# Performance work log

Hardware: AMD Instinct MI355X
Metric: run time of the kernel (lower is better)

## Reference

```python
import jax, jax.numpy as jnp
import numpy as np

D = 1024      # d_model
H = 4096      # d_hidden (attention head dim AND mlp width in this module)
V = 32000     # d_vocab
L = 4         # num_blocks
B = 2         # batch
S = 2048      # seq len == max_seq_length
SCALE = 1.0 / float(np.sqrt(D))  # note: original scales by sqrt(d_model), not sqrt(d_hidden)
EPS = 1e-5


def setup_inputs() -> dict:
    key = jax.random.key(0)
    ks = jax.random.split(key, 18)
    s = 0.02
    tokens = jax.random.randint(ks[0], (B, S), 0, V)
    tok_emb = jax.random.normal(ks[1], (V, D), dtype=jnp.float32) * s
    pos_emb = jax.random.normal(ks[2], (1, S, D), dtype=jnp.float32) * s
    # stacked per-block params [L, ...]
    Wq = jax.random.normal(ks[3], (L, D, H), dtype=jnp.float32) * s
    bq = jnp.zeros((L, H), jnp.float32)
    Wk = jax.random.normal(ks[4], (L, D, H), dtype=jnp.float32) * s
    bk = jnp.zeros((L, H), jnp.float32)
    Wv = jax.random.normal(ks[5], (L, D, H), dtype=jnp.float32) * s
    bv = jnp.zeros((L, H), jnp.float32)
    Wo = jax.random.normal(ks[6], (L, H, D), dtype=jnp.float32) * s
    bo = jnp.zeros((L, D), jnp.float32)
    Wup = jax.random.normal(ks[7], (L, D, H), dtype=jnp.float32) * s
    bup = jnp.zeros((L, H), jnp.float32)
    Wdn = jax.random.normal(ks[8], (L, H, D), dtype=jnp.float32) * s
    bdn = jnp.zeros((L, D), jnp.float32)
    ln_g = jnp.ones((D,), jnp.float32)
    ln_b = jnp.zeros((D,), jnp.float32)
    Wu = jax.random.normal(ks[9], (D, V), dtype=jnp.float32) * s
    bu = jnp.zeros((V,), jnp.float32)
    return dict(tokens=tokens, tok_emb=tok_emb, pos_emb=pos_emb,
                Wq=Wq, bq=bq, Wk=Wk, bk=bk, Wv=Wv, bv=bv, Wo=Wo, bo=bo,
                Wup=Wup, bup=bup, Wdn=Wdn, bdn=bdn,
                ln_g=ln_g, ln_b=ln_b, Wu=Wu, bu=bu)


def _forward(tokens, tok_emb, pos_emb, Wq, bq, Wk, bk, Wv, bv, Wo, bo,
             Wup, bup, Wdn, bdn, ln_g, ln_b, Wu, bu):
    seq = tokens.shape[1]
    x = tok_emb[tokens] + pos_emb[:, :seq, :]            # [B,S,D]
    mask = jnp.triu(jnp.full((seq, seq), -jnp.inf, jnp.float32), k=1)  # strict upper -inf

    def block(x, p):
        wq, _bq, wk, _bk, wv, _bv, wo, _bo, wup, _bup, wdn, _bdn = p
        Q = x @ wq + _bq                                  # [B,S,H]
        K = x @ wk + _bk
        Vv = x @ wv + _bv
        scores = jnp.einsum('bqh,bkh->bqk', Q, K) * SCALE + mask
        attn = jax.nn.softmax(scores, axis=-1)            # [B,S,S]
        x = x + jnp.einsum('bqk,bkh->bqh', attn, Vv) @ wo + _bo
        h = jax.nn.relu(x @ wup + _bup)
        x = x + h @ wdn + _bdn
        return x, None

    x, _ = jax.lax.scan(block, x, (Wq, bq, Wk, bk, Wv, bv, Wo, bo, Wup, bup, Wdn, bdn))
    mu = jnp.mean(x, axis=-1, keepdims=True)
    var = jnp.mean((x - mu) ** 2, axis=-1, keepdims=True)
    x = (x - mu) / jnp.sqrt(var + EPS) * ln_g + ln_b
    logits = x @ Wu + bu                                  # [B,S,V]
    return logits


def reference(tokens, tok_emb, pos_emb, Wq, bq, Wk, bk, Wv, bv, Wo, bo,
              Wup, bup, Wdn, bdn, ln_g, ln_b, Wu, bu):
    return _forward(tokens, tok_emb, pos_emb, Wq, bq, Wk, bk, Wv, bv, Wo, bo,
                    Wup, bup, Wdn, bdn, ln_g, ln_b, Wu, bu)
```

## Files before the change

kernel.cpp:

```cpp
#include <hip/hip_runtime.h>
#include <hip/hip_bf16.h>

typedef __bf16 bf16_t;
typedef __attribute__((ext_vector_type(8))) __bf16 bf16x8;
typedef __attribute__((ext_vector_type(4))) float f32x4;

#define D_MODEL 1024
#define H_DIM   4096
#define VOCAB   32000
#define NBLK    4
#define BATCH   2
#define SEQ     2048
#define NTOK    (BATCH*SEQ)
#define SCALE_QK (1.0f/32.0f)
#define LN_EPS  1e-5f

#define BM 128
#define BN 128
#define BK 32
#define GROUP_M 8
#define NXCD 8

__device__ __forceinline__ void gload16(const bf16_t* g, bf16_t* l) {
    __builtin_amdgcn_global_load_lds(
        (const __attribute__((address_space(1))) void*)g,
        (__attribute__((address_space(3))) void*)l,
        16, 0, 0);
}

__global__ void embed_kernel(const int* __restrict__ tokens,
                             const float* __restrict__ tok_emb,
                             const float* __restrict__ pos_emb,
                             float* __restrict__ x, bf16_t* __restrict__ xb) {
    int row = blockIdx.x;
    int s   = row & (SEQ - 1);
    int tok = tokens[row];
    const float* te = tok_emb + (size_t)tok * D_MODEL;
    const float* pe = pos_emb + (size_t)s * D_MODEL;
    int d = threadIdx.x * 4;
    float4 a = *(const float4*)(te + d);
    float4 p = *(const float4*)(pe + d);
    float4 r; r.x = a.x + p.x; r.y = a.y + p.y; r.z = a.z + p.z; r.w = a.w + p.w;
    *(float4*)(x + (size_t)row * D_MODEL + d) = r;
    union { bf16_t h[4]; unsigned long long u; } pk;
    pk.h[0] = (bf16_t)r.x; pk.h[1] = (bf16_t)r.y; pk.h[2] = (bf16_t)r.z; pk.h[3] = (bf16_t)r.w;
    *(unsigned long long*)(xb + (size_t)row * D_MODEL + d) = pk.u;
}

__global__ void transpose_cvt_kernel(const float* __restrict__ W, bf16_t* __restrict__ WT,
                                     int K, int N) {
    __shared__ float t[32][33];
    int k0 = blockIdx.y * 32, n0 = blockIdx.x * 32;
    int tx = threadIdx.x, ty = threadIdx.y;
    for (int i = ty; i < 32; i += 8) t[i][tx] = W[(size_t)(k0 + i) * N + n0 + tx];
    __syncthreads();
    for (int i = ty; i < 32; i += 8) WT[(size_t)(n0 + i) * K + k0 + tx] = (bf16_t)t[tx][i];
}

__global__ __launch_bounds__(512)
void gemm256_kernel(const bf16_t* __restrict__ A, const bf16_t* __restrict__ B,
                    const float* __restrict__ bias,
                    float* __restrict__ Cf, bf16_t* __restrict__ Cb,
                    int M, int N, int K, int ldb, int ldct, float scale, int flags) {
    extern __shared__ char lds[];

    const int nTM = M >> 8, nTN = N >> 8;
    const int nwg = nTM * nTN;
    int orig = blockIdx.x;
    const int q = nwg / NXCD, r = nwg % NXCD;
    const int xcd = orig % NXCD, idx = orig / NXCD;
    int wgid = (xcd < r ? xcd * (q + 1) : r * (q + 1) + (xcd - r) * q) + idx;
    const int tpg = GROUP_M * nTN;
    const int g   = wgid / tpg;
    const int rem = wgid % tpg;
    int gm = nTM - g * GROUP_M; if (gm > GROUP_M) gm = GROUP_M;
    const int mt = g * GROUP_M + rem % gm;
    const int nt = rem / gm;
    const int m0 = mt << 8, n0 = nt << 8;

    const int tid  = threadIdx.x;
    const int lane = tid & 63;
    const int wid  = tid >> 6;
    const int wr   = wid >> 2;
    const int wc   = wid & 3;

    const int srow = tid >> 3;
    const int scol = ((tid & 7) ^ (srow & 7)) << 3;
    const bf16_t* Ag = A + (size_t)(m0 + srow) * K   + scol;
    const bf16_t* Bg = B + (size_t)(n0 + srow) * ldb + scol;
    char* ldsw = lds + wid * 1024;

    const int lr  = lane & 15;
    const int kgb = (lane >> 4) * 16;
    const int xv  = (lane & 7) << 4;
    const int aoff = (wr * 128 + lr) * 128;
    const int boff = (wc * 64  + lr) * 128;

    f32x4 acc[8][4];
#pragma unroll
    for (int i = 0; i < 8; ++i)
#pragma unroll
        for (int j = 0; j < 4; ++j) acc[i][j] = (f32x4){0.f, 0.f, 0.f, 0.f};

    const int NT = K >> 6;

    auto stageA = [&](int t) {
#pragma unroll
        for (int j = 0; j < 4; ++j)
            gload16(Ag + (size_t)j * 64 * K + t * 64,
                    (bf16_t*)(ldsw + (t & 1) * 32768 + j * 8192));
    };
    auto stageBj = [&](int t, int j) {
        gload16(Bg + (size_t)j * 64 * ldb + t * 64,
                (bf16_t*)(ldsw + 65536 + (t % 3) * 32768 + j * 8192));
    };

    stageBj(0,0); stageBj(0,1); stageBj(0,2); stageBj(0,3); stageA(0);
    if (NT > 1) { stageBj(1,0); stageBj(1,1); stageBj(1,2); stageBj(1,3); stageA(1); }
    asm volatile("s_waitcnt vmcnt(8)" ::: "memory");
    __builtin_amdgcn_s_barrier();

    for (int s = 0; s < NT; ++s) {
        const char* Abase = lds + (s & 1) * 32768 + aoff;
        const char* Bbase = lds + 65536 + (s % 3) * 32768 + boff;
        const bool pf = (s + 2 < NT);
        const int klo = kgb ^ xv;
        const int khi = (64 + kgb) ^ xv;

        bf16x8 av[4], aw[4], bv[4];

#pragma unroll
        for (int i = 0; i < 4; ++i) av[i] = *(const bf16x8*)(Abase + i * 2048 + klo);
#pragma unroll
        for (int j = 0; j < 4; ++j) bv[j] = *(const bf16x8*)(Bbase + j * 2048 + klo);
        if (pf) { stageBj(s + 2, 0); stageBj(s + 2, 1); }
        __builtin_amdgcn_s_barrier();
        asm volatile("s_waitcnt lgkmcnt(0)" ::: "memory");
        __builtin_amdgcn_sched_barrier(0);
        __builtin_amdgcn_s_setprio(1);
#pragma unroll
        for (int i = 0; i < 4; ++i)
#pragma unroll
            for (int j = 0; j < 4; ++j)
                acc[i][j] = __builtin_amdgcn_mfma_f32_16x16x32_bf16(av[i], bv[j], acc[i][j], 0, 0, 0);
        __builtin_amdgcn_s_setprio(0);
        __builtin_amdgcn_s_barrier();

#pragma unroll
        for (int i = 0; i < 4; ++i) aw[i] = *(const bf16x8*)(Abase + (4 + i) * 2048 + klo);
        if (pf) { stageBj(s + 2, 2); stageBj(s + 2, 3); }
        __builtin_amdgcn_s_barrier();
        asm volatile("s_waitcnt lgkmcnt(0)" ::: "memory");
        __builtin_amdgcn_sched_barrier(0);
        __builtin_amdgcn_s_setprio(1);
#pragma unroll
        for (int i = 0; i < 4; ++i)
#pragma unroll
            for (int j = 0; j < 4; ++j)
                acc[4 + i][j] = __builtin_amdgcn_mfma_f32_16x16x32_bf16(aw[i], bv[j], acc[4 + i][j], 0, 0, 0);
        __builtin_amdgcn_s_setprio(0);
        __builtin_amdgcn_s_barrier();

#pragma unroll
        for (int i = 0; i < 4; ++i) av[i] = *(const bf16x8*)(Abase + i * 2048 + khi);
#pragma unroll
        for (int j = 0; j < 4; ++j) bv[j] = *(const bf16x8*)(Bbase + j * 2048 + khi);
        __builtin_amdgcn_s_barrier();
        asm volatile("s_waitcnt lgkmcnt(0)" ::: "memory");
        __builtin_amdgcn_sched_barrier(0);
        __builtin_amdgcn_s_setprio(1);
#pragma unroll
        for (int i = 0; i < 4; ++i)
#pragma unroll
            for (int j = 0; j < 4; ++j)
                acc[i][j] = __builtin_amdgcn_mfma_f32_16x16x32_bf16(av[i], bv[j], acc[i][j], 0, 0, 0);
        __builtin_amdgcn_s_setprio(0);
        __builtin_amdgcn_s_barrier();

#pragma unroll
        for (int i = 0; i < 4; ++i) aw[i] = *(const bf16x8*)(Abase + (4 + i) * 2048 + khi);
        asm volatile("s_waitcnt lgkmcnt(0)" ::: "memory");
        __builtin_amdgcn_sched_barrier(0);
        __builtin_amdgcn_s_barrier();
        if (pf) stageA(s + 2);
        __builtin_amdgcn_s_setprio(1);
#pragma unroll
        for (int i = 0; i < 4; ++i)
#pragma unroll
            for (int j = 0; j < 4; ++j)
                acc[4 + i][j] = __builtin_amdgcn_mfma_f32_16x16x32_bf16(aw[i], bv[j], acc[4 + i][j], 0, 0, 0);
        __builtin_amdgcn_s_setprio(0);
        if (pf) asm volatile("s_waitcnt vmcnt(8)" ::: "memory");
        else    asm volatile("s_waitcnt vmcnt(0)" ::: "memory");
        __builtin_amdgcn_sched_barrier(0);
        __builtin_amdgcn_s_barrier();
    }

    const int r0 = (lane >> 4) * 4;
    const int cc = lane & 15;
#pragma unroll
    for (int i = 0; i < 8; ++i) {
        const int growb = m0 + wr * 128 + i * 16 + r0;
#pragma unroll
        for (int j = 0; j < 4; ++j) {
            const int gcol = n0 + wc * 64 + j * 16 + cc;
            const float bv2 = bias ? bias[gcol] : 0.f;
#pragma unroll
            for (int r2 = 0; r2 < 4; ++r2) {
                const int grow = growb + r2;
                float v = acc[i][j][r2] * scale + bv2;
                if (flags & 1) v = fmaxf(v, 0.f);
                if (Cf) Cf[(size_t)grow * N + gcol] = v;
                if (Cb) {
                    if (flags & 8) Cb[(size_t)gcol * ldct + grow] = (bf16_t)v;
                    else           Cb[(size_t)grow * N + gcol]   = (bf16_t)v;
                }
            }
        }
    }
}

__global__ __launch_bounds__(256)
void gemm_bf16_kernel(const bf16_t* __restrict__ A, const bf16_t* __restrict__ B,
                      const float* __restrict__ bias, const float* __restrict__ resid,
                      float* __restrict__ Cf, bf16_t* __restrict__ Cb,
                      int M, int N, int K, int ldb, int ldct, float scale, int flags,
                      long bsA, long bsB, long bsC) {
    const int bidx = blockIdx.y;
    A += (size_t)bidx * bsA;
    B += (size_t)bidx * bsB;
    if (Cf) Cf += (size_t)bidx * bsC;
    if (Cb) Cb += (size_t)bidx * bsC;

    const int nTM = M / BM, nTN = N / BN;
    const int nwg = nTM * nTN;
    int orig = blockIdx.x;
    const int q = nwg / NXCD, r = nwg % NXCD;
    const int xcd = orig % NXCD, idx = orig / NXCD;
    int wgid = (xcd < r ? xcd * (q + 1) : r * (q + 1) + (xcd - r) * q) + idx;
    const int tpg = GROUP_M * nTN;
    const int g   = wgid / tpg;
    const int rem = wgid % tpg;
    int gm = nTM - g * GROUP_M; if (gm > GROUP_M) gm = GROUP_M;
    const int mt = g * GROUP_M + rem % gm;
    const int nt = rem / gm;

    const int m0 = mt * BM;
    const int n0 = nt * BN;
    if ((flags & 2) && n0 > m0 + BM - 1) return;
    const int Keff = (flags & 4) ? ((K < m0 + BM) ? K : (m0 + BM)) : K;

    __shared__ bf16_t As[BM * BK];
    __shared__ bf16_t Bs[BN * BK];

    const int tid  = threadIdx.x;
    const int lane = tid & 63;
    const int wid  = tid >> 6;
    const int wr   = (wid >> 1) * 64;
    const int wc   = (wid & 1) * 64;

    f32x4 acc[4][4];
#pragma unroll
    for (int i = 0; i < 4; ++i)
#pragma unroll
        for (int j = 0; j < 4; ++j)
            acc[i][j] = (f32x4){0.f, 0.f, 0.f, 0.f};

    const int r_in = lane >> 2;
    const int c8   = (lane & 3) * 8;
    const bf16_t* Ap = A + (size_t)(m0 + wid * 32 + r_in) * K   + c8;
    const bf16_t* Bp = B + (size_t)(n0 + wid * 32 + r_in) * ldb + c8;
    bf16_t* AsW = As + wid * 1024;
    bf16_t* BsW = Bs + wid * 1024;

    const int kg   = (lane >> 4) * 8;
    const int rsel = lane & 15;

    for (int k0 = 0; k0 < Keff; k0 += BK) {
        gload16(Ap + k0,                    AsW);
        gload16(Ap + k0 + (size_t)16 * K,   AsW + 512);
        gload16(Bp + k0,                    BsW);
        gload16(Bp + k0 + (size_t)16 * ldb, BsW + 512);
        __syncthreads();

        bf16x8 af[4], bfr[4];
#pragma unroll
        for (int i = 0; i < 4; ++i) {
            af[i]  = *(const bf16x8*)&As[(wr + i * 16 + rsel) * BK + kg];
            bfr[i] = *(const bf16x8*)&Bs[(wc + i * 16 + rsel) * BK + kg];
        }
#pragma unroll
        for (int i = 0; i < 4; ++i)
#pragma unroll
            for (int j = 0; j < 4; ++j)
                acc[i][j] = __builtin_amdgcn_mfma_f32_16x16x32_bf16(af[i], bfr[j], acc[i][j], 0, 0, 0);
        __syncthreads();
    }

    const int r0 = (lane >> 4) * 4;
    const int cc = lane & 15;
#pragma unroll
    for (int i = 0; i < 4; ++i) {
        const int growb = m0 + wr + i * 16 + r0;
#pragma unroll
        for (int j = 0; j < 4; ++j) {
            const int gcol = n0 + wc + j * 16 + cc;
            const float bv = bias ? bias[gcol] : 0.f;
#pragma unroll
            for (int r2 = 0; r2 < 4; ++r2) {
                const int grow = growb + r2;
                float v = acc[i][j][r2] * scale + bv;
                if (resid) v += resid[(size_t)grow * N + gcol];
                if (flags & 1) v = fmaxf(v, 0.f);
                if (Cf) Cf[(size_t)grow * N + gcol] = v;
                if (Cb) {
                    if (flags & 8) Cb[(size_t)gcol * ldct + grow] = (bf16_t)v;
                    else           Cb[(size_t)grow * N + gcol]   = (bf16_t)v;
                }
            }
        }
    }
}

__global__ __launch_bounds__(256)
void gemmsk_kernel(const bf16_t* __restrict__ A, const bf16_t* __restrict__ B,
                   float* __restrict__ Cp, int M, int N, int K, int ldb, int Kc) {
    const int chunk = blockIdx.y;
    const int koff  = chunk * Kc;
    Cp += (size_t)chunk * M * N;

    const int nTM = M / BM, nTN = N / BN;
    const int nwg = nTM * nTN;
    int orig = blockIdx.x;
    const int q = nwg / NXCD, r = nwg % NXCD;
    const int xcd = orig % NXCD, idx = orig / NXCD;
    int wgid = (xcd < r ? xcd * (q + 1) : r * (q + 1) + (xcd - r) * q) + idx;
    const int tpg = GROUP_M * nTN;
    const int g   = wgid / tpg;
    const int rem = wgid % tpg;
    int gm = nTM - g * GROUP_M; if (gm > GROUP_M) gm = GROUP_M;
    const int mt = g * GROUP_M + rem % gm;
    const int nt = rem / gm;
    const int m0 = mt * BM;
    const int n0 = nt * BN;

    __shared__ bf16_t As[BM * BK];
    __shared__ bf16_t Bs[BN * BK];

    const int tid  = threadIdx.x;
    const int lane = tid & 63;
    const int wid  = tid >> 6;
    const int wr   = (wid >> 1) * 64;
    const int wc   = (wid & 1) * 64;

    f32x4 acc[4][4];
#pragma unroll
    for (int i = 0; i < 4; ++i)
#pragma unroll
        for (int j = 0; j < 4; ++j)
            acc[i][j] = (f32x4){0.f, 0.f, 0.f, 0.f};

    const int r_in = lane >> 2;
    const int c8   = (lane & 3) * 8;
    const bf16_t* Ap = A + (size_t)(m0 + wid * 32 + r_in) * K   + koff + c8;
    const bf16_t* Bp = B + (size_t)(n0 + wid * 32 + r_in) * ldb + koff + c8;
    bf16_t* AsW = As + wid * 1024;
    bf16_t* BsW = Bs + wid * 1024;

    const int kg   = (lane >> 4) * 8;
    const int rsel = lane & 15;

    for (int k0 = 0; k0 < Kc; k0 += BK) {
        gload16(Ap + k0,                    AsW);
        gload16(Ap + k0 + (size_t)16 * K,   AsW + 512);
        gload16(Bp + k0,                    BsW);
        gload16(Bp + k0 + (size_t)16 * ldb, BsW + 512);
        __syncthreads();

        bf16x8 af[4], bfr[4];
#pragma unroll
        for (int i = 0; i < 4; ++i) {
            af[i]  = *(const bf16x8*)&As[(wr + i * 16 + rsel) * BK + kg];
            bfr[i] = *(const bf16x8*)&Bs[(wc + i * 16 + rsel) * BK + kg];
        }
#pragma unroll
        for (int i = 0; i < 4; ++i)
#pragma unroll
            for (int j = 0; j < 4; ++j)
                acc[i][j] = __builtin_amdgcn_mfma_f32_16x16x32_bf16(af[i], bfr[j], acc[i][j], 0, 0, 0);
        __syncthreads();
    }

    const int r0 = (lane >> 4) * 4;
    const int cc = lane & 15;
#pragma unroll
    for (int i = 0; i < 4; ++i) {
        const int growb = m0 + wr + i * 16 + r0;
#pragma unroll
        for (int j = 0; j < 4; ++j) {
            const int gcol = n0 + wc + j * 16 + cc;
#pragma unroll
            for (int r2 = 0; r2 < 4; ++r2)
                Cp[(size_t)(growb + r2) * N + gcol] = acc[i][j][r2];
        }
    }
}

__global__ void reduce4_kernel(const float* __restrict__ Cp, const float* __restrict__ bias,
                               float* __restrict__ x, bf16_t* __restrict__ xb, int N) {
    const int row = blockIdx.x;
    const int col = threadIdx.x * 4;
    const size_t base = (size_t)row * N + col;
    const size_t cs = (size_t)gridDim.x * N;
    float4 v0 = *(const float4*)(Cp + base);
    float4 v1 = *(const float4*)(Cp + base + cs);
    float4 v2 = *(const float4*)(Cp + base + 2 * cs);
    float4 v3 = *(const float4*)(Cp + base + 3 * cs);
    float4 bb = *(const float4*)(bias + col);
    float4 rr = *(const float4*)(x + base);
    float4 o;
    o.x = v0.x + v1.x + v2.x + v3.x + bb.x + rr.x;
    o.y = v0.y + v1.y + v2.y + v3.y + bb.y + rr.y;
    o.z = v0.z + v1.z + v2.z + v3.z + bb.z + rr.z;
    o.w = v0.w + v1.w + v2.w + v3.w + bb.w + rr.w;
    *(float4*)(x + base) = o;
    union { bf16_t h[4]; unsigned long long u; } pk;
    pk.h[0] = (bf16_t)o.x; pk.h[1] = (bf16_t)o.y; pk.h[2] = (bf16_t)o.z; pk.h[3] = (bf16_t)o.w;
    *(unsigned long long*)(xb + base) = pk.u;
}

__global__ void softmax_kernel(const float* __restrict__ sc, bf16_t* __restrict__ pr) {
    int row = blockIdx.x;
    int q   = row & (SEQ - 1);
    const float* s = sc + (size_t)row * SEQ;
    bf16_t*      p = pr + (size_t)row * SEQ;
    int n   = q + 1;
    int tid = threadIdx.x;
    __shared__ float red[4];
    float lmax = -3.4e38f;
    for (int k = tid; k < n; k += 256) lmax = fmaxf(lmax, s[k]);
    for (int o = 32; o > 0; o >>= 1) lmax = fmaxf(lmax, __shfl_down(lmax, o, 64));
    if ((tid & 63) == 0) red[tid >> 6] = lmax;
    __syncthreads();
    float gmax = fmaxf(fmaxf(red[0], red[1]), fmaxf(red[2], red[3]));
    __syncthreads();
    float lsum = 0.f;
    for (int k = tid; k < n; k += 256) lsum += __expf(s[k] - gmax);
    for (int o = 32; o > 0; o >>= 1) lsum += __shfl_down(lsum, o, 64);
    if ((tid & 63) == 0) red[tid >> 6] = lsum;
    __syncthreads();
    float inv = 1.f / (red[0] + red[1] + red[2] + red[3]);
    for (int k = tid; k < SEQ; k += 256) {
        float v = (k < n) ? __expf(s[k] - gmax) * inv : 0.f;
        p[k] = (bf16_t)v;
    }
}

__global__ void ln_kernel(const float* __restrict__ x, const float* __restrict__ g,
                          const float* __restrict__ b, bf16_t* __restrict__ o) {
    int row = blockIdx.x;
    int tid = threadIdx.x;
    const float* xr = x + (size_t)row * D_MODEL;
    int d = tid * 4;
    float4 v = *(const float4*)(xr + d);
    float s  = v.x + v.y + v.z + v.w;
    float s2 = v.x * v.x + v.y * v.y + v.z * v.z + v.w * v.w;
    __shared__ float rs[4], rs2[4];
    for (int of = 32; of > 0; of >>= 1) { s += __shfl_down(s, of, 64); s2 += __shfl_down(s2, of, 64); }
    if ((tid & 63) == 0) { rs[tid >> 6] = s; rs2[tid >> 6] = s2; }
    __syncthreads();
    float mean = (rs[0] + rs[1] + rs[2] + rs[3]) * (1.f / D_MODEL);
    float var  = (rs2[0] + rs2[1] + rs2[2] + rs2[3]) * (1.f / D_MODEL) - mean * mean;
    float rstd = rsqrtf(var + LN_EPS);
    float4 gg = *(const float4*)(g + d);
    float4 bb = *(const float4*)(b + d);
    union { bf16_t h[4]; unsigned long long u; } pk;
    pk.h[0] = (bf16_t)((v.x - mean) * rstd * gg.x + bb.x);
    pk.h[1] = (bf16_t)((v.y - mean) * rstd * gg.y + bb.y);
    pk.h[2] = (bf16_t)((v.z - mean) * rstd * gg.z + bb.z);
    pk.h[3] = (bf16_t)((v.w - mean) * rstd * gg.w + bb.w);
    *(unsigned long long*)(o + (size_t)row * D_MODEL + d) = pk.u;
}

extern "C" void kernel_launch(void* const* d_in, const int* in_sizes, int n_in,
                              void* d_out, int out_size, void* d_ws, size_t ws_size,
                              hipStream_t stream) {
    const int*   tokens  = (const int*)d_in[0];
    const float* tok_emb = (const float*)d_in[1];
    const float* pos_emb = (const float*)d_in[2];
    const float* Wq = (const float*)d_in[3];
    const float* bq = (const float*)d_in[4];
    const float* Wk = (const float*)d_in[5];
    const float* bk = (const float*)d_in[6];
    const float* Wv = (const float*)d_in[7];
    const float* bv = (const float*)d_in[8];
    const float* Wo = (const float*)d_in[9];
    const float* bo = (const float*)d_in[10];
    const float* Wup = (const float*)d_in[11];
    const float* bup = (const float*)d_in[12];
    const float* Wdn = (const float*)d_in[13];
    const float* bdn = (const float*)d_in[14];
    const float* ln_g = (const float*)d_in[15];
    const float* ln_b = (const float*)d_in[16];
    const float* Wu = (const float*)d_in[17];
    const float* bu = (const float*)d_in[18];
    float* out = (float*)d_out;

    (void)hipFuncSetAttribute((const void*)gemm256_kernel,
                              hipFuncAttributeMaxDynamicSharedMemorySize, 163840);

    char* ws = (char*)d_ws;
    size_t off = 0;
    auto alloc = [&](size_t bytes) -> void* {
        void* p = ws + off; off += (bytes + 255) & ~(size_t)255; return p;
    };
    float*  x   = (float*)alloc((size_t)NTOK * D_MODEL * 4);
    bf16_t* xb  = (bf16_t*)alloc((size_t)NTOK * D_MODEL * 2);
    bf16_t* Qb  = (bf16_t*)alloc((size_t)NTOK * H_DIM * 2);
    bf16_t* Kb  = (bf16_t*)alloc((size_t)NTOK * H_DIM * 2);
    bf16_t* Vt  = (bf16_t*)alloc((size_t)NTOK * H_DIM * 2);
    float*  sc  = (float*)alloc((size_t)BATCH * SEQ * SEQ * 4);
    bf16_t* pr  = (bf16_t*)alloc((size_t)BATCH * SEQ * SEQ * 2);
    bf16_t* ao  = (bf16_t*)alloc((size_t)NTOK * H_DIM * 2);
    bf16_t* hb  = (bf16_t*)alloc((size_t)NTOK * H_DIM * 2);
    bf16_t* xln = (bf16_t*)alloc((size_t)NTOK * D_MODEL * 2);
    bf16_t* WT  = (bf16_t*)alloc((size_t)VOCAB * D_MODEL * 2);
    float*  Cp  = (float*)alloc((size_t)4 * NTOK * D_MODEL * 4);

    auto gemm = [&](const bf16_t* A, const bf16_t* B, const float* bias, const float* resid,
                    float* Cf, bf16_t* Cb, int M, int N, int K, int ldb, int ldct,
                    float scale, int flags, long bsA = 0, long bsB = 0, long bsC = 0,
                    int gy = 1) {
        int nwg = (N / BN) * (M / BM);
        gemm_bf16_kernel<<<dim3(nwg, gy), 256, 0, stream>>>(A, B, bias, resid, Cf, Cb,
                                                            M, N, K, ldb, ldct, scale, flags,
                                                            bsA, bsB, bsC);
    };
    auto gemm256 = [&](const bf16_t* A, const bf16_t* B, const float* bias,
                       float* Cf, bf16_t* Cb, int M, int N, int K, int ldb, int ldct,
                       float scale, int flags) {
        int nwg = (N / 256) * (M / 256);
        gemm256_kernel<<<nwg, 512, 163840, stream>>>(A, B, bias, Cf, Cb,
                                                     M, N, K, ldb, ldct, scale, flags);
    };
    auto gemmsk = [&](const bf16_t* A, const bf16_t* B, const float* bias,
                      int M, int N, int K) {
        int nwg = (N / BN) * (M / BM);
        gemmsk_kernel<<<dim3(nwg, 4), 256, 0, stream>>>(A, B, Cp, M, N, K, K, K / 4);
        reduce4_kernel<<<M, N / 4, 0, stream>>>(Cp, bias, x, xb, N);
    };
    auto tcvt = [&](const float* W, bf16_t* T, int K, int N) {
        transpose_cvt_kernel<<<dim3(N / 32, K / 32), dim3(32, 8), 0, stream>>>(W, T, K, N);
    };

    embed_kernel<<<NTOK, 256, 0, stream>>>(tokens, tok_emb, pos_emb, x, xb);

    for (int l = 0; l < NBLK; ++l) {
        const float* wq = Wq + (size_t)l * D_MODEL * H_DIM;
        const float* wk = Wk + (size_t)l * D_MODEL * H_DIM;
        const float* wv = Wv + (size_t)l * D_MODEL * H_DIM;
        const float* wo = Wo + (size_t)l * H_DIM * D_MODEL;
        const float* wup = Wup + (size_t)l * D_MODEL * H_DIM;
        const float* wdn = Wdn + (size_t)l * H_DIM * D_MODEL;
        const float* bql = bq + (size_t)l * H_DIM;
        const float* bkl = bk + (size_t)l * H_DIM;
        const float* bvl = bv + (size_t)l * H_DIM;
        const float* bol = bo + (size_t)l * D_MODEL;
        const float* bupl = bup + (size_t)l * H_DIM;
        const float* bdnl = bdn + (size_t)l * D_MODEL;

        tcvt(wq, WT, D_MODEL, H_DIM);
        gemm256(xb, WT, bql, nullptr, Qb, NTOK, H_DIM, D_MODEL, D_MODEL, 0, 1.f, 0);
        tcvt(wk, WT, D_MODEL, H_DIM);
        gemm256(xb, WT, bkl, nullptr, Kb, NTOK, H_DIM, D_MODEL, D_MODEL, 0, 1.f, 0);
        tcvt(wv, WT, D_MODEL, H_DIM);
        gemm256(xb, WT, bvl, nullptr, Vt, NTOK, H_DIM, D_MODEL, D_MODEL, NTOK, 1.f, 8);

        gemm(Qb, Kb, nullptr, nullptr, sc, nullptr, SEQ, SEQ, H_DIM, H_DIM, 0,
             SCALE_QK, 2, (long)SEQ * H_DIM, (long)SEQ * H_DIM, (long)SEQ * SEQ, BATCH);

        softmax_kernel<<<NTOK, 256, 0, stream>>>(sc, pr);

        gemm(pr, Vt, nullptr, nullptr, nullptr, ao, SEQ, H_DIM, SEQ, NTOK, 0,
             1.f, 4, (long)SEQ * SEQ, (long)SEQ, (long)SEQ * H_DIM, BATCH);

        tcvt(wo, WT, H_DIM, D_MODEL);
        gemmsk(ao, WT, bol, NTOK, D_MODEL, H_DIM);

        tcvt(wup, WT, D_MODEL, H_DIM);
        gemm256(xb, WT, bupl, nullptr, hb, NTOK, H_DIM, D_MODEL, D_MODEL, 0, 1.f, 1);

        tcvt(wdn, WT, H_DIM, D_MODEL);
        gemmsk(hb, WT, bdnl, NTOK, D_MODEL, H_DIM);
    }

    ln_kernel<<<NTOK, 256, 0, stream>>>(x, ln_g, ln_b, xln);
    tcvt(Wu, WT, D_MODEL, VOCAB);
    gemm256(xln, WT, bu, out, nullptr, NTOK, VOCAB, D_MODEL, D_MODEL, 0, 1.f, 0);
}
```

Before: 2.953 ms.

## Replace 256x256 pipelined GEMM with 256x128 double-buffered batched kernel

Swaps the hand-scheduled 256x256 tile GEMM (triple-buffered B, 160KB dynamic LDS, setprio and sched barriers) for a simpler 256x128 tile kernel with static double-buffered LDS and BK=32, launch-bounded for more resident waves. The new kernel supports batching and causal K truncation, so it also takes over the attention P@V product from the older 128x128 GEMM. The aim is higher occupancy and better load balance, but it gives up the deep software pipelining and cuts per-tile reuse. It also adds a full __syncthreads every 32-wide K step.

```diff
diff --git a/kernel.cpp b/kernel.cpp
--- a/kernel.cpp
+++ b/kernel.cpp
@@ -57,158 +57,99 @@
     for (int i = ty; i < 32; i += 8) WT[(size_t)(n0 + i) * K + k0 + tx] = (bf16_t)t[tx][i];
 }
 
-__global__ __launch_bounds__(512)
-void gemm256_kernel(const bf16_t* __restrict__ A, const bf16_t* __restrict__ B,
-                    const float* __restrict__ bias,
-                    float* __restrict__ Cf, bf16_t* __restrict__ Cb,
-                    int M, int N, int K, int ldb, int ldct, float scale, int flags) {
-    extern __shared__ char lds[];
-
-    const int nTM = M >> 8, nTN = N >> 8;
+__global__ __launch_bounds__(512, 6)
+void gemmd_kernel(const bf16_t* __restrict__ A, const bf16_t* __restrict__ B,
+                  const float* __restrict__ bias,
+                  float* __restrict__ Cf, bf16_t* __restrict__ Cb,
+                  int M, int N, int K, int ldb, int ldct, float scale, int flags,
+                  long bsA, long bsB, long bsC) {
+    __shared__ bf16_t As[2][256 * 32];
+    __shared__ bf16_t Bs[2][128 * 32];
+    const int bidx = blockIdx.y;
+    A += (size_t)bidx * bsA;
+    B += (size_t)bidx * bsB;
+    if (Cf) Cf += (size_t)bidx * bsC;
+    if (Cb) Cb += (size_t)bidx * bsC;
+
+    const int nTM = M >> 8, nTN = N >> 7;
     const int nwg = nTM * nTN;
     int orig = blockIdx.x;
     const int q = nwg / NXCD, r = nwg % NXCD;
     const int xcd = orig % NXCD, idx = orig / NXCD;
     int wgid = (xcd < r ? xcd * (q + 1) : r * (q + 1) + (xcd - r) * q) + idx;
     const int tpg = GROUP_M * nTN;
-    const int g   = wgid / tpg;
+    const int g2  = wgid / tpg;
     const int rem = wgid % tpg;
-    int gm = nTM - g * GROUP_M; if (gm > GROUP_M) gm = GROUP_M;
-    const int mt = g * GROUP_M + rem % gm;
+    int gm = nTM - g2 * GROUP_M; if (gm > GROUP_M) gm = GROUP_M;
+    const int mt = g2 * GROUP_M + rem % gm;
     const int nt = rem / gm;
-    const int m0 = mt << 8, n0 = nt << 8;
+    const int m0 = mt << 8, n0 = nt << 7;
+    const int Keff = (flags & 4) ? ((K < m0 + 256) ? K : (m0 + 256)) : K;
+    const int NT = Keff >> 5;
 
     const int tid  = threadIdx.x;
     const int lane = tid & 63;
     const int wid  = tid >> 6;
-    const int wr   = wid >> 2;
-    const int wc   = wid & 3;
-
-    const int srow = tid >> 3;
-    const int scol = ((tid & 7) ^ (srow & 7)) << 3;
-    const bf16_t* Ag = A + (size_t)(m0 + srow) * K   + scol;
-    const bf16_t* Bg = B + (size_t)(n0 + srow) * ldb + scol;
-    char* ldsw = lds + wid * 1024;
-
-    const int lr  = lane & 15;
-    const int kgb = (lane >> 4) * 16;
-    const int xv  = (lane & 7) << 4;
-    const int aoff = (wr * 128 + lr) * 128;
-    const int boff = (wc * 64  + lr) * 128;
-
-    f32x4 acc[8][4];
-#pragma unroll
-    for (int i = 0; i < 8; ++i)
+    const int wr   = wid >> 1;
+    const int wc   = wid & 1;
+
+    const int sr   = tid >> 2;
+    const int scol = (((tid & 3) ^ ((tid >> 3) & 3)) << 3);
+    const bf16_t* Ag0 = A + (size_t)(m0 + sr) * K + scol;
+    const bf16_t* Ag1 = A + (size_t)(m0 + 128 + sr) * K + scol;
+    const bf16_t* Bg  = B + (size_t)(n0 + sr) * ldb + scol;
+
+    const int lr = lane & 15;
+    const int gc = lane >> 4;
+    const int ch = (gc ^ ((lr >> 1) & 3)) << 4;
+    const int abase = (wr * 64 + lr) * 64 + ch;
+    const int bbase = (wc * 64 + lr) * 64 + ch;
+
+    f32x4 acc[4][4];
+#pragma unroll
+    for (int i = 0; i < 4; ++i)
 #pragma unroll
         for (int j = 0; j < 4; ++j) acc[i][j] = (f32x4){0.f, 0.f, 0.f, 0.f};
 
-    const int NT = K >> 6;
-
-    auto stageA = [&](int t) {
-#pragma unroll
-        for (int j = 0; j < 4; ++j)
-            gload16(Ag + (size_t)j * 64 * K + t * 64,
-                    (bf16_t*)(ldsw + (t & 1) * 32768 + j * 8192));
+    auto stage = [&](int t) {
+        const int b = t & 1;
+        gload16(Ag0 + t * 32, &As[b][wid * 512]);
+        gload16(Ag1 + t * 32, &As[b][4096 + wid * 512]);
+        gload16(Bg  + t * 32, &Bs[b][wid * 512]);
     };
-    auto stageBj = [&](int t, int j) {
-        gload16(Bg + (size_t)j * 64 * ldb + t * 64,
-                (bf16_t*)(ldsw + 65536 + (t % 3) * 32768 + j * 8192));
-    };
-
-    stageBj(0,0); stageBj(0,1); stageBj(0,2); stageBj(0,3); stageA(0);
-    if (NT > 1) { stageBj(1,0); stageBj(1,1); stageBj(1,2); stageBj(1,3); stageA(1); }
-    asm volatile("s_waitcnt vmcnt(8)" ::: "memory");
-    __builtin_amdgcn_s_barrier();
-
-    for (int s = 0; s < NT; ++s) {
-        const char* Abase = lds + (s & 1) * 32768 + aoff;
-        const char* Bbase = lds + 65536 + (s % 3) * 32768 + boff;
-        const bool pf = (s + 2 < NT);
-        const int klo = kgb ^ xv;
-        const int khi = (64 + kgb) ^ xv;
-
-        bf16x8 av[4], aw[4], bv[4];
-
-#pragma unroll
-        for (int i = 0; i < 4; ++i) av[i] = *(const bf16x8*)(Abase + i * 2048 + klo);
-#pragma unroll
-        for (int j = 0; j < 4; ++j) bv[j] = *(const bf16x8*)(Bbase + j * 2048 + klo);
-        if (pf) { stageBj(s + 2, 0); stageBj(s + 2, 1); }
-        __builtin_amdgcn_s_barrier();
-        asm volatile("s_waitcnt lgkmcnt(0)" ::: "memory");
-        __builtin_amdgcn_sched_barrier(0);
-        __builtin_amdgcn_s_setprio(1);
+
+    stage(0);
+    __syncthreads();
+    for (int t = 0; t < NT; ++t) {
+        if (t + 1 < NT) stage(t + 1);
+        const char* Ab = (const char*)As[t & 1] + abase;
+        const char* Bb = (const char*)Bs[t & 1] + bbase;
+        bf16x8 af[4], bfv[4];
+#pragma unroll
+        for (int i = 0; i < 4; ++i) af[i]  = *(const bf16x8*)(Ab + i * 1024);
+#pragma unroll
+        for (int j = 0; j < 4; ++j) bfv[j] = *(const bf16x8*)(Bb + j * 1024);
 #pragma unroll
         for (int i = 0; i < 4; ++i)
 #pragma unroll
             for (int j = 0; j < 4; ++j)
-                acc[i][j] = __builtin_amdgcn_mfma_f32_16x16x32_bf16(av[i], bv[j], acc[i][j], 0, 0, 0);
-        __builtin_amdgcn_s_setprio(0);
-        __builtin_amdgcn_s_barrier();
-
-#pragma unroll
-        for (int i = 0; i < 4; ++i) aw[i] = *(const bf16x8*)(Abase + (4 + i) * 2048 + klo);
-        if (pf) { stageBj(s + 2, 2); stageBj(s + 2, 3); }
-        __builtin_amdgcn_s_barrier();
-        asm volatile("s_waitcnt lgkmcnt(0)" ::: "memory");
-        __builtin_amdgcn_sched_barrier(0);
-        __builtin_amdgcn_s_setprio(1);
-#pragma unroll
-        for (int i = 0; i < 4; ++i)
-#pragma unroll
-            for (int j = 0; j < 4; ++j)
-                acc[4 + i][j] = __builtin_amdgcn_mfma_f32_16x16x32_bf16(aw[i], bv[j], acc[4 + i][j], 0, 0, 0);
-        __builtin_amdgcn_s_setprio(0);
-        __builtin_amdgcn_s_barrier();
-
-#pragma unroll
-        for (int i = 0; i < 4; ++i) av[i] = *(const bf16x8*)(Abase + i * 2048 + khi);
-#pragma unroll
-        for (int j = 0; j < 4; ++j) bv[j] = *(const bf16x8*)(Bbase + j * 2048 + khi);
-        __builtin_amdgcn_s_barrier();
-        asm volatile("s_waitcnt lgkmcnt(0)" ::: "memory");
-        __builtin_amdgcn_sched_barrier(0);
-        __builtin_amdgcn_s_setprio(1);
-#pragma unroll
-        for (int i = 0; i < 4; ++i)
-#pragma unroll
-            for (int j = 0; j < 4; ++j)
-                acc[i][j] = __builtin_amdgcn_mfma_f32_16x16x32_bf16(av[i], bv[j], acc[i][j], 0, 0, 0);
-        __builtin_amdgcn_s_setprio(0);
-        __builtin_amdgcn_s_barrier();
-
-#pragma unroll
-        for (int i = 0; i < 4; ++i) aw[i] = *(const bf16x8*)(Abase + (4 + i) * 2048 + khi);
-        asm volatile("s_waitcnt lgkmcnt(0)" ::: "memory");
-        __builtin_amdgcn_sched_barrier(0);
-        __builtin_amdgcn_s_barrier();
-        if (pf) stageA(s + 2);
-        __builtin_amdgcn_s_setprio(1);
-#pragma unroll
-        for (int i = 0; i < 4; ++i)
-#pragma unroll
-            for (int j = 0; j < 4; ++j)
-                acc[4 + i][j] = __builtin_amdgcn_mfma_f32_16x16x32_bf16(aw[i], bv[j], acc[4 + i][j], 0, 0, 0);
-        __builtin_amdgcn_s_setprio(0);
-        if (pf) asm volatile("s_waitcnt vmcnt(8)" ::: "memory");
-        else    asm volatile("s_waitcnt vmcnt(0)" ::: "memory");
-        __builtin_amdgcn_sched_barrier(0);
-        __builtin_amdgcn_s_barrier();
+                acc[i][j] = __builtin_amdgcn_mfma_f32_16x16x32_bf16(af[i], bfv[j], acc[i][j], 0, 0, 0);
+        __syncthreads();
     }
 
     const int r0 = (lane >> 4) * 4;
     const int cc = lane & 15;
 #pragma unroll
-    for (int i = 0; i < 8; ++i) {
-        const int growb = m0 + wr * 128 + i * 16 + r0;
+    for (int i = 0; i < 4; ++i) {
+        const int growb = m0 + wr * 64 + i * 16 + r0;
 #pragma unroll
         for (int j = 0; j < 4; ++j) {
             const int gcol = n0 + wc * 64 + j * 16 + cc;
-            const float bv2 = bias ? bias[gcol] : 0.f;
+            const float bv = bias ? bias[gcol] : 0.f;
 #pragma unroll
             for (int r2 = 0; r2 < 4; ++r2) {
                 const int grow = growb + r2;
-                float v = acc[i][j][r2] * scale + bv2;
+                float v = acc[i][j][r2] * scale + bv;
                 if (flags & 1) v = fmaxf(v, 0.f);
                 if (Cf) Cf[(size_t)grow * N + gcol] = v;
                 if (Cb) {
@@ -506,9 +447,6 @@
     const float* bu = (const float*)d_in[18];
     float* out = (float*)d_out;
 
-    (void)hipFuncSetAttribute((const void*)gemm256_kernel,
-                              hipFuncAttributeMaxDynamicSharedMemorySize, 163840);
-
     char* ws = (char*)d_ws;
     size_t off = 0;
     auto alloc = [&](size_t bytes) -> void* {
@@ -536,12 +474,14 @@
                                                             M, N, K, ldb, ldct, scale, flags,
                                                             bsA, bsB, bsC);
     };
-    auto gemm256 = [&](const bf16_t* A, const bf16_t* B, const float* bias,
-                       float* Cf, bf16_t* Cb, int M, int N, int K, int ldb, int ldct,
-                       float scale, int flags) {
-        int nwg = (N / 256) * (M / 256);
-        gemm256_kernel<<<nwg, 512, 163840, stream>>>(A, B, bias, Cf, Cb,
-                                                     M, N, K, ldb, ldct, scale, flags);
+    auto gemmd = [&](const bf16_t* A, const bf16_t* B, const float* bias,
+                     float* Cf, bf16_t* Cb, int M, int N, int K, int ldb, int ldct,
+                     float scale, int flags, long bsA = 0, long bsB = 0, long bsC = 0,
+                     int gy = 1) {
+        int nwg = (N / 128) * (M / 256);
+        gemmd_kernel<<<dim3(nwg, gy), 512, 0, stream>>>(A, B, bias, Cf, Cb,
+                                                        M, N, K, ldb, ldct, scale, flags,
+                                                        bsA, bsB, bsC);
     };
     auto gemmsk = [&](const bf16_t* A, const bf16_t* B, const float* bias,
                       int M, int N, int K) {
@@ -570,25 +510,25 @@
         const float* bdnl = bdn + (size_t)l * D_MODEL;
 
         tcvt(wq, WT, D_MODEL, H_DIM);
-        gemm256(xb, WT, bql, nullptr, Qb, NTOK, H_DIM, D_MODEL, D_MODEL, 0, 1.f, 0);
+        gemmd(xb, WT, bql, nullptr, Qb, NTOK, H_DIM, D_MODEL, D_MODEL, 0, 1.f, 0);
         tcvt(wk, WT, D_MODEL, H_DIM);
-        gemm256(xb, WT, bkl, nullptr, Kb, NTOK, H_DIM, D_MODEL, D_MODEL, 0, 1.f, 0);
+        gemmd(xb, WT, bkl, nullptr, Kb, NTOK, H_DIM, D_MODEL, D_MODEL, 0, 1.f, 0);
         tcvt(wv, WT, D_MODEL, H_DIM);
-        gemm256(xb, WT, bvl, nullptr, Vt, NTOK, H_DIM, D_MODEL, D_MODEL, NTOK, 1.f, 8);
+        gemmd(xb, WT, bvl, nullptr, Vt, NTOK, H_DIM, D_MODEL, D_MODEL, NTOK, 1.f, 8);
 
         gemm(Qb, Kb, nullptr, nullptr, sc, nullptr, SEQ, SEQ, H_DIM, H_DIM, 0,
              SCALE_QK, 2, (long)SEQ * H_DIM, (long)SEQ * H_DIM, (long)SEQ * SEQ, BATCH);
 
         softmax_kernel<<<NTOK, 256, 0, stream>>>(sc, pr);
 
-        gemm(pr, Vt, nullptr, nullptr, nullptr, ao, SEQ, H_DIM, SEQ, NTOK, 0,
-             1.f, 4, (long)SEQ * SEQ, (long)SEQ, (long)SEQ * H_DIM, BATCH);
+        gemmd(pr, Vt, nullptr, nullptr, ao, SEQ, H_DIM, SEQ, NTOK, 0,
+              1.f, 4, (long)SEQ * SEQ, (long)SEQ, (long)SEQ * H_DIM, BATCH);
 
         tcvt(wo, WT, H_DIM, D_MODEL);
         gemmsk(ao, WT, bol, NTOK, D_MODEL, H_DIM);
 
         tcvt(wup, WT, D_MODEL, H_DIM);
-        gemm256(xb, WT, bupl, nullptr, hb, NTOK, H_DIM, D_MODEL, D_MODEL, 0, 1.f, 1);
+        gemmd(xb, WT, bupl, nullptr, hb, NTOK, H_DIM, D_MODEL, D_MODEL, 0, 1.f, 1);
 
         tcvt(wdn, WT, H_DIM, D_MODEL);
         gemmsk(hb, WT, bdnl, NTOK, D_MODEL, H_DIM);
@@ -596,5 +536,5 @@
 
     ln_kernel<<<NTOK, 256, 0, stream>>>(x, ln_g, ln_b, xln);
     tcvt(Wu, WT, D_MODEL, VOCAB);
-    gemm256(xln, WT, bu, out, nullptr, NTOK, VOCAB, D_MODEL, D_MODEL, 0, 1.f, 0);
-}
+    gemmd(xln, WT, bu, out, nullptr, NTOK, VOCAB, D_MODEL, D_MODEL, 0, 1.f, 0);
+}
```

Result: slower. 6.717 ms (+127.5%).

## Replace split-K with smaller-tile full-K GEMM fusing bias and residual epilogue

Applied to the files above, without the earlier changes.

The Wo and Wdn projections previously ran a 4-way split-K GEMM that wrote fp32 partials to a workspace, then a separate reduction kernel summed them and added bias and residual. Now a single kernel uses 128x64 tiles over the full K and performs the bias add, residual update and bf16 copy in its epilogue. This removes the large partial-sum write/read traffic and one kernel launch per projection. The trade-off is a smaller output tile with lower data reuse and longer serial K loops per workgroup.

```diff
diff --git a/kernel.cpp b/kernel.cpp
--- a/kernel.cpp
+++ b/kernel.cpp
@@ -323,13 +323,11 @@
 }
 
 __global__ __launch_bounds__(256)
-void gemmsk_kernel(const bf16_t* __restrict__ A, const bf16_t* __restrict__ B,
-                   float* __restrict__ Cp, int M, int N, int K, int ldb, int Kc) {
-    const int chunk = blockIdx.y;
-    const int koff  = chunk * Kc;
-    Cp += (size_t)chunk * M * N;
-
-    const int nTM = M / BM, nTN = N / BN;
+void gemm_nk_kernel(const bf16_t* __restrict__ A, const bf16_t* __restrict__ B,
+                    const float* __restrict__ bias,
+                    float* __restrict__ x, bf16_t* __restrict__ xb,
+                    int M, int N, int K) {
+    const int nTM = M / 128, nTN = N / 64;
     const int nwg = nTM * nTN;
     int orig = blockIdx.x;
     const int q = nwg / NXCD, r = nwg % NXCD;
@@ -341,52 +339,52 @@
     int gm = nTM - g * GROUP_M; if (gm > GROUP_M) gm = GROUP_M;
     const int mt = g * GROUP_M + rem % gm;
     const int nt = rem / gm;
-    const int m0 = mt * BM;
-    const int n0 = nt * BN;
-
-    __shared__ bf16_t As[BM * BK];
-    __shared__ bf16_t Bs[BN * BK];
+    const int m0 = mt * 128;
+    const int n0 = nt * 64;
+
+    __shared__ bf16_t As[128 * BK];
+    __shared__ bf16_t Bs[64 * BK];
 
     const int tid  = threadIdx.x;
     const int lane = tid & 63;
     const int wid  = tid >> 6;
     const int wr   = (wid >> 1) * 64;
-    const int wc   = (wid & 1) * 64;
-
-    f32x4 acc[4][4];
+    const int wc   = (wid & 1) * 32;
+
+    f32x4 acc[4][2];
 #pragma unroll
     for (int i = 0; i < 4; ++i)
 #pragma unroll
-        for (int j = 0; j < 4; ++j)
+        for (int j = 0; j < 2; ++j)
             acc[i][j] = (f32x4){0.f, 0.f, 0.f, 0.f};
 
     const int r_in = lane >> 2;
     const int c8   = (lane & 3) * 8;
-    const bf16_t* Ap = A + (size_t)(m0 + wid * 32 + r_in) * K   + koff + c8;
-    const bf16_t* Bp = B + (size_t)(n0 + wid * 32 + r_in) * ldb + koff + c8;
+    const bf16_t* Ap = A + (size_t)(m0 + wid * 32 + r_in) * K + c8;
+    const bf16_t* Bp = B + (size_t)(n0 + wid * 16 + r_in) * K + c8;
     bf16_t* AsW = As + wid * 1024;
-    bf16_t* BsW = Bs + wid * 1024;
+    bf16_t* BsW = Bs + wid * 512;
 
     const int kg   = (lane >> 4) * 8;
     const int rsel = lane & 15;
 
-    for (int k0 = 0; k0 < Kc; k0 += BK) {
-        gload16(Ap + k0,                    AsW);
-        gload16(Ap + k0 + (size_t)16 * K,   AsW + 512);
-        gload16(Bp + k0,                    BsW);
-        gload16(Bp + k0 + (size_t)16 * ldb, BsW + 512);
+    for (int k0 = 0; k0 < K; k0 += BK) {
+        gload16(Ap + k0,                  AsW);
+        gload16(Ap + k0 + (size_t)16 * K, AsW + 512);
+        gload16(Bp + k0,                  BsW);
         __syncthreads();
 
-        bf16x8 af[4], bfr[4];
-#pragma unroll
-        for (int i = 0; i < 4; ++i) {
+        bf16x8 af[4], bfr[2];
+#pragma unroll
+        for (int i = 0; i < 4; ++i)
             af[i]  = *(const bf16x8*)&As[(wr + i * 16 + rsel) * BK + kg];
-            bfr[i] = *(const bf16x8*)&Bs[(wc + i * 16 + rsel) * BK + kg];
-        }
-#pragma unroll
-        for (int i = 0; i < 4; ++i)
-#pragma unroll
-            for (int j = 0; j < 4; ++j)
+#pragma unroll
+        for (int j = 0; j < 2; ++j)
+            bfr[j] = *(const bf16x8*)&Bs[(wc + j * 16 + rsel) * BK + kg];
+#pragma unroll
+        for (int i = 0; i < 4; ++i)
+#pragma unroll
+            for (int j = 0; j < 2; ++j)
                 acc[i][j] = __builtin_amdgcn_mfma_f32_16x16x32_bf16(af[i], bfr[j], acc[i][j], 0, 0, 0);
         __syncthreads();
     }
@@ -397,36 +395,19 @@
     for (int i = 0; i < 4; ++i) {
         const int growb = m0 + wr + i * 16 + r0;
 #pragma unroll
-        for (int j = 0; j < 4; ++j) {
+        for (int j = 0; j < 2; ++j) {
             const int gcol = n0 + wc + j * 16 + cc;
-#pragma unroll
-            for (int r2 = 0; r2 < 4; ++r2)
-                Cp[(size_t)(growb + r2) * N + gcol] = acc[i][j][r2];
+            const float bv = bias[gcol];
+#pragma unroll
+            for (int r2 = 0; r2 < 4; ++r2) {
+                const int grow = growb + r2;
+                const size_t off = (size_t)grow * N + gcol;
+                float v = acc[i][j][r2] + bv + x[off];
+                x[off]  = v;
+                xb[off] = (bf16_t)v;
+            }
         }
     }
-}
-
-__global__ void reduce4_kernel(const float* __restrict__ Cp, const float* __restrict__ bias,
-                               float* __restrict__ x, bf16_t* __restrict__ xb, int N) {
-    const int row = blockIdx.x;
-    const int col = threadIdx.x * 4;
-    const size_t base = (size_t)row * N + col;
-    const size_t cs = (size_t)gridDim.x * N;
-    float4 v0 = *(const float4*)(Cp + base);
-    float4 v1 = *(const float4*)(Cp + base + cs);
-    float4 v2 = *(const float4*)(Cp + base + 2 * cs);
-    float4 v3 = *(const float4*)(Cp + base + 3 * cs);
-    float4 bb = *(const float4*)(bias + col);
-    float4 rr = *(const float4*)(x + base);
-    float4 o;
-    o.x = v0.x + v1.x + v2.x + v3.x + bb.x + rr.x;
-    o.y = v0.y + v1.y + v2.y + v3.y + bb.y + rr.y;
-    o.z = v0.z + v1.z + v2.z + v3.z + bb.z + rr.z;
-    o.w = v0.w + v1.w + v2.w + v3.w + bb.w + rr.w;
-    *(float4*)(x + base) = o;
-    union { bf16_t h[4]; unsigned long long u; } pk;
-    pk.h[0] = (bf16_t)o.x; pk.h[1] = (bf16_t)o.y; pk.h[2] = (bf16_t)o.z; pk.h[3] = (bf16_t)o.w;
-    *(unsigned long long*)(xb + base) = pk.u;
 }
 
 __global__ void softmax_kernel(const float* __restrict__ sc, bf16_t* __restrict__ pr) {
@@ -525,7 +506,6 @@
     bf16_t* hb  = (bf16_t*)alloc((size_t)NTOK * H_DIM * 2);
     bf16_t* xln = (bf16_t*)alloc((size_t)NTOK * D_MODEL * 2);
     bf16_t* WT  = (bf16_t*)alloc((size_t)VOCAB * D_MODEL * 2);
-    float*  Cp  = (float*)alloc((size_t)4 * NTOK * D_MODEL * 4);
 
     auto gemm = [&](const bf16_t* A, const bf16_t* B, const float* bias, const float* resid,
                     float* Cf, bf16_t* Cb, int M, int N, int K, int ldb, int ldct,
@@ -543,11 +523,10 @@
         gemm256_kernel<<<nwg, 512, 163840, stream>>>(A, B, bias, Cf, Cb,
                                                      M, N, K, ldb, ldct, scale, flags);
     };
-    auto gemmsk = [&](const bf16_t* A, const bf16_t* B, const float* bias,
+    auto gemmnk = [&](const bf16_t* A, const bf16_t* B, const float* bias,
                       int M, int N, int K) {
-        int nwg = (N / BN) * (M / BM);
-        gemmsk_kernel<<<dim3(nwg, 4), 256, 0, stream>>>(A, B, Cp, M, N, K, K, K / 4);
-        reduce4_kernel<<<M, N / 4, 0, stream>>>(Cp, bias, x, xb, N);
+        int nwg = (N / 64) * (M / 128);
+        gemm_nk_kernel<<<nwg, 256, 0, stream>>>(A, B, bias, x, xb, M, N, K);
     };
     auto tcvt = [&](const float* W, bf16_t* T, int K, int N) {
         transpose_cvt_kernel<<<dim3(N / 32, K / 32), dim3(32, 8), 0, stream>>>(W, T, K, N);
@@ -585,13 +564,13 @@
              1.f, 4, (long)SEQ * SEQ, (long)SEQ, (long)SEQ * H_DIM, BATCH);
 
         tcvt(wo, WT, H_DIM, D_MODEL);
-        gemmsk(ao, WT, bol, NTOK, D_MODEL, H_DIM);
+        gemmnk(ao, WT, bol, NTOK, D_MODEL, H_DIM);
 
         tcvt(wup, WT, D_MODEL, H_DIM);
         gemm256(xb, WT, bupl, nullptr, hb, NTOK, H_DIM, D_MODEL, D_MODEL, 0, 1.f, 1);
 
         tcvt(wdn, WT, H_DIM, D_MODEL);
-        gemmsk(hb, WT, bdnl, NTOK, D_MODEL, H_DIM);
+        gemmnk(hb, WT, bdnl, NTOK, D_MODEL, H_DIM);
     }
 
     ln_kernel<<<NTOK, 256, 0, stream>>>(x, ln_g, ln_b, xln);
```

After: 2.964 ms. No clear change (+0.4%).
